# Kernel tuning notes

Measured on AMD Instinct MI355X. Metric: run time of the kernel, lower is better.

## Reference

```python
import jax, jax.numpy as jnp
import numpy as np

B, H, W, C, NH, WS, SS = 32, 56, 56, 128, 4, 7, 3
L = H * W
N = WS * WS
HD = C // NH
EPS = 1e-5


def _rel_pos_index():
    coords = np.stack(np.meshgrid(np.arange(WS), np.arange(WS), indexing='ij'))  # (2,ws,ws)
    flat = coords.reshape(2, -1)  # (2,N)
    rel = flat[:, :, None] - flat[:, None, :]  # (2,N,N)
    rel = rel.transpose(1, 2, 0).astype(np.int64)
    rel[..., 0] += WS - 1
    rel[..., 1] += WS - 1
    rel[..., 0] *= 2 * WS - 1
    return jnp.asarray(rel.sum(-1), dtype=jnp.int32)  # (N,N)


def setup_inputs() -> dict:
    key = jax.random.key(0)
    ks = jax.random.split(key, 8)
    s = 0.02
    return {
        'x': jax.random.normal(ks[0], (B, L, C), jnp.float32),
        'norm1_g': jnp.ones((C,), jnp.float32),
        'norm1_b': jnp.zeros((C,), jnp.float32),
        'qkv_w': jax.random.normal(ks[1], (3 * C, C), jnp.float32) * s,
        'qkv_b': jnp.zeros((3 * C,), jnp.float32),
        'rpb_table': jax.random.normal(ks[2], ((2 * WS - 1) ** 2, NH), jnp.float32) * s,
        'proj_w': jax.random.normal(ks[3], (C, C), jnp.float32) * s,
        'proj_b': jnp.zeros((C,), jnp.float32),
        'norm2_g': jnp.ones((C,), jnp.float32),
        'norm2_b': jnp.zeros((C,), jnp.float32),
        'fc1_w': jax.random.normal(ks[4], (4 * C, C), jnp.float32) * s,
        'fc1_b': jnp.zeros((4 * C,), jnp.float32),
        'fc2_w': jax.random.normal(ks[5], (C, 4 * C), jnp.float32) * s,
        'fc2_b': jnp.zeros((C,), jnp.float32),
        'rel_idx': _rel_pos_index(),
    }


def _ln(h, g, b):
    mu = jnp.mean(h, axis=-1, keepdims=True)
    var = jnp.mean((h - mu) ** 2, axis=-1, keepdims=True)
    return (h - mu) * jax.lax.rsqrt(var + EPS) * g + b


def reference(x, norm1_g, norm1_b, qkv_w, qkv_b, rpb_table, proj_w, proj_b,
              norm2_g, norm2_b, fc1_w, fc1_b, fc2_w, fc2_b, rel_idx):
    nHw, nWw = H // WS, W // WS
    scale = HD ** (-0.5)

    shortcut = x
    h = _ln(x, norm1_g, norm1_b).reshape(B, H, W, C)
    # cyclic shift
    h = jnp.roll(h, shift=(-SS, -SS), axis=(1, 2))
    # window partition -> (B*nW, N, C)
    w = h.reshape(B, nHw, WS, nWw, WS, C).transpose(0, 1, 3, 2, 4, 5)
    w = w.reshape(B * nHw * nWw, N, C)

    qkv = w @ qkv_w.T + qkv_b  # (Bw, N, 3C)
    q, k, v = jnp.split(qkv, 3, axis=-1)
    q = q.reshape(-1, N, NH, HD).transpose(0, 2, 1, 3)  # (Bw, nh, N, hd)
    k = k.reshape(-1, N, NH, HD).transpose(0, 2, 1, 3)
    v = v.reshape(-1, N, NH, HD).transpose(0, 2, 1, 3)

    attn = jnp.einsum('bhnd,bhmd->bhnm', q * scale, k)
    bias = rpb_table[rel_idx.reshape(-1)].reshape(N, N, NH).transpose(2, 0, 1)  # (nh,N,N)
    attn = jax.nn.softmax(attn + bias[None], axis=-1)

    out = jnp.einsum('bhnm,bhmd->bhnd', attn, v)
    out = out.transpose(0, 2, 1, 3).reshape(-1, N, C)
    out = out @ proj_w.T + proj_b

    # window reverse + un-shift
    out = out.reshape(B, nHw, nWw, WS, WS, C).transpose(0, 1, 3, 2, 4, 5)
    out = out.reshape(B, H, W, C)
    out = jnp.roll(out, shift=(SS, SS), axis=(1, 2)).reshape(B, L, C)

    x = shortcut + out
    h2 = _ln(x, norm2_g, norm2_b)
    mlp = jax.nn.gelu(h2 @ fc1_w.T + fc1_b, approximate=False) @ fc2_w.T + fc2_b
    return x + mlp
```

## Files before the change

### kernel.cpp

```cpp
#include <hip/hip_runtime.h>

typedef unsigned short ushort_t;
typedef unsigned int uint_t;

typedef __bf16 bf16x8 __attribute__((ext_vector_type(8)));
typedef float f32x4 __attribute__((ext_vector_type(4)));

static __device__ __forceinline__ float bf2f(ushort_t h) {
    return __uint_as_float(((uint_t)h) << 16);
}
static __device__ __forceinline__ ushort_t f2bf(float f) {
    uint_t u = __float_as_uint(f);
    u = u + 0x7FFFu + ((u >> 16) & 1u);
    return (ushort_t)(u >> 16);
}
static __device__ __forceinline__ uint_t pkbf(float lo, float hi) {
    uint_t a = __float_as_uint(lo) + 0x8000u;
    uint_t b = __float_as_uint(hi) + 0x8000u;
    return __builtin_amdgcn_perm(b, a, 0x07060302u);
}

#define BB 32
#define HH 56
#define WW_ 56
#define CC 128
#define NHEAD 4
#define WS 7
#define SS 3
#define LL (HH * WW_)
#define NTOK (BB * LL)
#define NWIN (BB * 64)
#define NN 49
#define HD 32
#define PLS 40
#define VTS 72

static __device__ __forceinline__ int win2tok(int wid) {
    int win = wid / NN, t = wid - win * NN;
    int bb = win >> 6, wrem = win & 63;
    int wi = wrem >> 3, wj = wrem & 7;
    int ti = t / WS, tj = t - ti * WS;
    int hh = wi * WS + ti + SS; if (hh >= HH) hh -= HH;
    int ww = wj * WS + tj + SS; if (ww >= WW_) ww -= WW_;
    return bb * LL + hh * WW_ + ww;
}

__global__ __launch_bounds__(256) void prep_all(
    const float* __restrict__ qkv_w, const float* __restrict__ proj_w,
    const float* __restrict__ fc1_w, const float* __restrict__ fc2_w,
    ushort_t* __restrict__ dst,
    const float* __restrict__ rpb, const int* __restrict__ rel_idx,
    float* __restrict__ bias) {
    int b = blockIdx.x;
    if (b < 768) {
        int i = b * 256 + threadIdx.x;
        const float* src;
        int off;
        if (i < 49152)        { src = qkv_w;  off = i; }
        else if (i < 65536)   { src = proj_w; off = i - 49152; }
        else if (i < 131072)  { src = fc1_w;  off = i - 65536; }
        else                  { src = fc2_w;  off = i - 131072; }
        dst[i] = f2bf(src[off]);
    } else {
        int h = b - 768;
        for (int idx = threadIdx.x; idx < 4096; idx += 256) {
            int i = idx >> 6, j = idx & 63;
            float v = 0.f;
            if (i < NN && j < NN)
                v = rpb[(size_t)rel_idx[i * NN + j] * NHEAD + h];
            bias[h * 4096 + idx] = v;
        }
    }
}

__global__ __launch_bounds__(256) void swin_fused(
    const float* __restrict__ x, const float* __restrict__ g1,
    const float* __restrict__ b1ln, const ushort_t* __restrict__ wq,
    const float* __restrict__ qkv_b, const float* __restrict__ bias,
    const ushort_t* __restrict__ wp, const float* __restrict__ proj_b,
    const float* __restrict__ g2, const float* __restrict__ b2,
    const ushort_t* __restrict__ w1, const float* __restrict__ fc1b,
    const ushort_t* __restrict__ w2, const float* __restrict__ bias2,
    float* __restrict__ out) {
    __shared__ __align__(16) ushort_t U[16384];
    __shared__ __align__(16) ushort_t HV[NHEAD][32 * VTS];
    __shared__ float MRm[64];
    __shared__ float MRs[64];
    const int tid = threadIdx.x;
    const int wave = tid >> 6;
    const int lane = tid & 63;
    const int l16 = lane & 15;
    const int quad = lane >> 4;
    const int h = wave;
    const int win = blockIdx.x;
    const int wn = wave * 32;
    const float scale = 0.17677669529663687f;

    ushort_t* XLN = U;
    char* QK = (char*)(U + h * 4096);
    ushort_t* PL = U + h * 4096;
    ushort_t* VT = HV[h];
    ushort_t* AH = U;
    ushort_t* PS = (ushort_t*)HV;

    {
        int row = tid >> 2;
        int ch0 = (tid & 3) * 32;
        int t = (row < NN) ? row : 0;
        int gtok = win2tok(win * NN + t);
        const float* xp = x + (size_t)gtok * CC + ch0;
        float v[32];
        float s = 0.f, sq = 0.f;
        #pragma unroll
        for (int i = 0; i < 4; ++i) {
            float4 a0 = *(const float4*)(xp + i * 8);
            float4 a1 = *(const float4*)(xp + i * 8 + 4);
            v[i * 8 + 0] = a0.x; v[i * 8 + 1] = a0.y;
            v[i * 8 + 2] = a0.z; v[i * 8 + 3] = a0.w;
            v[i * 8 + 4] = a1.x; v[i * 8 + 5] = a1.y;
            v[i * 8 + 6] = a1.z; v[i * 8 + 7] = a1.w;
            #pragma unroll
            for (int j = 0; j < 8; ++j) { s += v[i * 8 + j]; sq += v[i * 8 + j] * v[i * 8 + j]; }
        }
        s += __shfl_xor(s, 1);  sq += __shfl_xor(sq, 1);
        s += __shfl_xor(s, 2);  sq += __shfl_xor(sq, 2);
        float mean = s * (1.0f / 128.0f);
        float var = sq * (1.0f / 128.0f) - mean * mean;
        float rstd = rsqrtf(var + 1e-5f);
        #pragma unroll
        for (int i = 0; i < 4; ++i) {
            ushort_t tmp[8];
            #pragma unroll
            for (int j = 0; j < 8; ++j) {
                int c = ch0 + i * 8 + j;
                tmp[j] = f2bf((v[i * 8 + j] - mean) * rstd * g1[c] + b1ln[c]);
            }
            *(uint4*)&XLN[row * 136 + ch0 + i * 8] = *(const uint4*)tmp;
        }
    }
    __syncthreads();

    bf16x8 tf[4][4];
    #pragma unroll
    for (int kk = 0; kk < 4; ++kk)
        #pragma unroll
        for (int i = 0; i < 4; ++i)
            tf[kk][i] = *(const bf16x8*)&XLN[(16 * i + l16) * 136 + kk * 32 + quad * 8];
    __syncthreads();

    #pragma unroll
    for (int j = 0; j < 2; ++j) {
        f32x4 s1[4];
        #pragma unroll
        for (int i = 0; i < 4; ++i)
            s1[i] = (f32x4){0.f, 0.f, 0.f, 0.f};
        #pragma unroll
        for (int kk = 0; kk < 4; ++kk) {
            bf16x8 wf = *(const bf16x8*)&wq[(size_t)(h * 32 + 16 * j + l16) * 128 + kk * 32 + quad * 8];
            #pragma unroll
            for (int i = 0; i < 4; ++i)
                s1[i] = __builtin_amdgcn_mfma_f32_16x16x32_bf16(wf, tf[kk][i], s1[i], 0, 0, 0);
        }
        float4 bv = *(const float4*)&qkv_b[h * 32 + 16 * j + quad * 4];
        #pragma unroll
        for (int i = 0; i < 4; ++i) {
            uint2 pk;
            pk.x = pkbf((s1[i][0] + bv.x) * scale, (s1[i][1] + bv.y) * scale);
            pk.y = pkbf((s1[i][2] + bv.z) * scale, (s1[i][3] + bv.w) * scale);
            int row = 16 * i + l16;
            *(uint2*)(QK + row * 128 + ((32 * j + 8 * quad) ^ ((row & 7) << 4))) = pk;
        }
    }
    #pragma unroll
    for (int j = 0; j < 2; ++j) {
        f32x4 s1[4];
        #pragma unroll
        for (int i = 0; i < 4; ++i)
            s1[i] = (f32x4){0.f, 0.f, 0.f, 0.f};
        #pragma unroll
        for (int kk = 0; kk < 4; ++kk) {
            bf16x8 wf = *(const bf16x8*)&wq[(size_t)(128 + h * 32 + 16 * j + l16) * 128 + kk * 32 + quad * 8];
            #pragma unroll
            for (int i = 0; i < 4; ++i)
                s1[i] = __builtin_amdgcn_mfma_f32_16x16x32_bf16(wf, tf[kk][i], s1[i], 0, 0, 0);
        }
        float4 bv = *(const float4*)&qkv_b[128 + h * 32 + 16 * j + quad * 4];
        #pragma unroll
        for (int i = 0; i < 4; ++i) {
            uint2 pk;
            pk.x = pkbf(s1[i][0] + bv.x, s1[i][1] + bv.y);
            pk.y = pkbf(s1[i][2] + bv.z, s1[i][3] + bv.w);
            int row = 16 * i + l16;
            *(uint2*)(QK + row * 128 + ((64 + 32 * j + 8 * quad) ^ ((row & 7) << 4))) = pk;
        }
    }
    #pragma unroll
    for (int j = 0; j < 2; ++j) {
        f32x4 sv[4];
        #pragma unroll
        for (int i = 0; i < 4; ++i)
            sv[i] = (f32x4){0.f, 0.f, 0.f, 0.f};
        #pragma unroll
        for (int kk = 0; kk < 4; ++kk) {
            bf16x8 wf = *(const bf16x8*)&wq[(size_t)(256 + h * 32 + 16 * j + l16) * 128 + kk * 32 + quad * 8];
            #pragma unroll
            for (int i = 0; i < 4; ++i)
                sv[i] = __builtin_amdgcn_mfma_f32_16x16x32_bf16(tf[kk][i], wf, sv[i], 0, 0, 0);
        }
        float bvv = qkv_b[256 + h * 32 + 16 * j + l16];
        #pragma unroll
        for (int i = 0; i < 4; ++i) {
            uint2 pk;
            pk.x = pkbf(sv[i][0] + bvv, sv[i][1] + bvv);
            pk.y = pkbf(sv[i][2] + bvv, sv[i][3] + bvv);
            *(uint2*)&VT[(16 * j + l16) * VTS + 16 * i + quad * 4] = pk;
        }
    }

    f32x4 s[4][4];
    {
        bf16x8 qa[4], kb[4];
        #pragma unroll
        for (int t = 0; t < 4; ++t) {
            int row = 16 * t + l16;
            int swz = (row & 7) << 4;
            qa[t] = *(const bf16x8*)(QK + row * 128 + ((16 * quad) ^ swz));
            kb[t] = *(const bf16x8*)(QK + row * 128 + ((64 + 16 * quad) ^ swz));
        }
        #pragma unroll
        for (int mi = 0; mi < 4; ++mi)
            #pragma unroll
            for (int ni = 0; ni < 4; ++ni) {
                f32x4 z = {0.f, 0.f, 0.f, 0.f};
                s[mi][ni] = __builtin_amdgcn_mfma_f32_16x16x32_bf16(qa[mi], kb[ni], z, 0, 0, 0);
            }
    }

    const float* bh = bias + h * 4096;
    #pragma unroll
    for (int mi = 0; mi < 4; ++mi)
        #pragma unroll
        for (int ni = 0; ni < 4; ++ni)
            #pragma unroll
            for (int r = 0; r < 4; ++r)
                s[mi][ni][r] += bh[(16 * mi + quad * 4 + r) * 64 + 16 * ni + l16];

    #pragma unroll
    for (int mi = 0; mi < 4; ++mi)
        #pragma unroll
        for (int r = 0; r < 4; ++r) {
            float e0 = __expf(s[mi][0][r]);
            float e1 = __expf(s[mi][1][r]);
            float e2 = __expf(s[mi][2][r]);
            float e3 = (l16 == 0) ? __expf(s[mi][3][r]) : 0.f;
            float sum = (e0 + e1) + (e2 + e3);
            sum += __shfl_xor(sum, 1);
            sum += __shfl_xor(sum, 2);
            sum += __shfl_xor(sum, 4);
            sum += __shfl_xor(sum, 8);
            float inv = __builtin_amdgcn_rcpf(sum);
            s[mi][0][r] = e0 * inv;
            s[mi][1][r] = e1 * inv;
            s[mi][2][r] = e2 * inv;
            s[mi][3][r] = e3 * inv;
        }

    uint2 pP[4][4];
    #pragma unroll
    for (int mi = 0; mi < 4; ++mi)
        #pragma unroll
        for (int ni = 0; ni < 4; ++ni) {
            pP[mi][ni].x = pkbf(s[mi][ni][0], s[mi][ni][1]);
            pP[mi][ni].y = pkbf(s[mi][ni][2], s[mi][ni][3]);
        }

    f32x4 o[2][4];
    #pragma unroll
    for (int k0 = 0; k0 < 64; k0 += 32) {
        int nb = k0 >> 4;
        #pragma unroll
        for (int mi = 0; mi < 4; ++mi)
            #pragma unroll
            for (int nn = 0; nn < 2; ++nn) {
                uint2 pk = pP[mi][nb + nn];
                int base = (16 * mi + quad * 4) * PLS + 16 * nn + l16;
                PL[base] = (ushort_t)pk.x;
                PL[base + PLS] = (ushort_t)(pk.x >> 16);
                PL[base + 2 * PLS] = (ushort_t)pk.y;
                PL[base + 3 * PLS] = (ushort_t)(pk.y >> 16);
            }
        bf16x8 va[2], pb[4];
        #pragma unroll
        for (int it = 0; it < 2; ++it)
            va[it] = *(const bf16x8*)&VT[(16 * it + l16) * VTS + k0 + quad * 8];
        #pragma unroll
        for (int jt = 0; jt < 4; ++jt)
            pb[jt] = *(const bf16x8*)&PL[(16 * jt + l16) * PLS + quad * 8];
        #pragma unroll
        for (int it = 0; it < 2; ++it)
            #pragma unroll
            for (int jt = 0; jt < 4; ++jt) {
                if (k0 == 0) {
                    f32x4 z = {0.f, 0.f, 0.f, 0.f};
                    o[it][jt] = __builtin_amdgcn_mfma_f32_16x16x32_bf16(va[it], pb[jt], z, 0, 0, 0);
                } else {
                    o[it][jt] = __builtin_amdgcn_mfma_f32_16x16x32_bf16(va[it], pb[jt], o[it][jt], 0, 0, 0);
                }
            }
    }
    __syncthreads();

    #pragma unroll
    for (int jt = 0; jt < 4; ++jt) {
        int m = 16 * jt + l16;
        #pragma unroll
        for (int it = 0; it < 2; ++it) {
            ushort4 st;
            st.x = f2bf(o[it][jt][0]);
            st.y = f2bf(o[it][jt][1]);
            st.z = f2bf(o[it][jt][2]);
            st.w = f2bf(o[it][jt][3]);
            *(ushort4*)&AH[m * 136 + h * HD + 16 * it + quad * 4] = st;
        }
    }
    __syncthreads();

    {
        f32x4 pa[2][4];
        #pragma unroll
        for (int j = 0; j < 2; ++j)
            #pragma unroll
            for (int i = 0; i < 4; ++i)
                pa[j][i] = (f32x4){0.f, 0.f, 0.f, 0.f};
        #pragma unroll
        for (int kk = 0; kk < 4; ++kk) {
            bf16x8 af[4];
            #pragma unroll
            for (int i = 0; i < 4; ++i)
                af[i] = *(const bf16x8*)&AH[(16 * i + l16) * 136 + kk * 32 + quad * 8];
            #pragma unroll
            for (int j = 0; j < 2; ++j) {
                bf16x8 wf = *(const bf16x8*)&wp[(size_t)(wn + 16 * j + l16) * 128 + kk * 32 + quad * 8];
                #pragma unroll
                for (int i = 0; i < 4; ++i)
                    pa[j][i] = __builtin_amdgcn_mfma_f32_16x16x32_bf16(wf, af[i], pa[j][i], 0, 0, 0);
            }
        }
        #pragma unroll
        for (int j = 0; j < 2; ++j) {
            float4 bv = *(const float4*)&proj_b[wn + 16 * j + quad * 4];
            #pragma unroll
            for (int i = 0; i < 4; ++i) {
                uint2 pk;
                pk.x = pkbf(pa[j][i][0] + bv.x, pa[j][i][1] + bv.y);
                pk.y = pkbf(pa[j][i][2] + bv.z, pa[j][i][3] + bv.w);
                *(uint2*)&PS[(16 * i + l16) * 136 + wn + 16 * j + quad * 4] = pk;
            }
        }
    }
    __syncthreads();

    {
        int row = tid >> 2;
        int ch0 = (tid & 3) * 32;
        int t = (row < NN) ? row : 0;
        int gtok = win2tok(win * NN + t);
        const float* xp = x + (size_t)gtok * CC + ch0;
        float v[32];
        float s2 = 0.f, sq = 0.f;
        #pragma unroll
        for (int i = 0; i < 4; ++i) {
            float4 a0 = *(const float4*)(xp + i * 8);
            float4 a1 = *(const float4*)(xp + i * 8 + 4);
            ushort4 p0 = *(const ushort4*)&PS[row * 136 + ch0 + i * 8];
            ushort4 p1 = *(const ushort4*)&PS[row * 136 + ch0 + i * 8 + 4];
            v[i * 8 + 0] = a0.x + bf2f(p0.x); v[i * 8 + 1] = a0.y + bf2f(p0.y);
            v[i * 8 + 2] = a0.z + bf2f(p0.z); v[i * 8 + 3] = a0.w + bf2f(p0.w);
            v[i * 8 + 4] = a1.x + bf2f(p1.x); v[i * 8 + 5] = a1.y + bf2f(p1.y);
            v[i * 8 + 6] = a1.z + bf2f(p1.z); v[i * 8 + 7] = a1.w + bf2f(p1.w);
            #pragma unroll
            for (int j = 0; j < 8; ++j) { s2 += v[i * 8 + j]; sq += v[i * 8 + j] * v[i * 8 + j]; }
        }
        s2 += __shfl_xor(s2, 1);  sq += __shfl_xor(sq, 1);
        s2 += __shfl_xor(s2, 2);  sq += __shfl_xor(sq, 2);
        float mean = s2 * (1.0f / 128.0f);
        float var = sq * (1.0f / 128.0f) - mean * mean;
        float rstd = rsqrtf(var + 1e-5f);
        if ((tid & 3) == 0) {
            MRm[row] = mean;
            MRs[row] = (var + 1e-5f) * rstd;
        }
        #pragma unroll
        for (int i = 0; i < 4; ++i) {
            ushort_t tmp[8];
            #pragma unroll
            for (int j = 0; j < 8; ++j) {
                int c = ch0 + i * 8 + j;
                tmp[j] = f2bf((v[i * 8 + j] - mean) * rstd * g2[c] + b2[c]);
            }
            *(uint4*)&AH[row * 136 + ch0 + i * 8] = *(const uint4*)tmp;
        }
    }
    __syncthreads();

    f32x4 acc2[2][4];
    #pragma unroll
    for (int j = 0; j < 2; ++j)
        #pragma unroll
        for (int i = 0; i < 4; ++i)
            acc2[j][i] = (f32x4){0.f, 0.f, 0.f, 0.f};

    for (int c = 0; c < 4; ++c) {
        f32x4 s1[2][4];
        #pragma unroll
        for (int j = 0; j < 2; ++j)
            #pragma unroll
            for (int i = 0; i < 4; ++i)
                s1[j][i] = (f32x4){0.f, 0.f, 0.f, 0.f};
        #pragma unroll
        for (int kk = 0; kk < 4; ++kk) {
            bf16x8 hf[4];
            #pragma unroll
            for (int i = 0; i < 4; ++i)
                hf[i] = *(const bf16x8*)&AH[(16 * i + l16) * 136 + kk * 32 + quad * 8];
            #pragma unroll
            for (int j = 0; j < 2; ++j) {
                bf16x8 wf = *(const bf16x8*)&w1[(size_t)(c * 128 + wn + 16 * j + l16) * 128 + kk * 32 + quad * 8];
                #pragma unroll
                for (int i = 0; i < 4; ++i)
                    s1[j][i] = __builtin_amdgcn_mfma_f32_16x16x32_bf16(wf, hf[i], s1[j][i], 0, 0, 0);
            }
        }
        uint2 pk[2][4];
        #pragma unroll
        for (int j = 0; j < 2; ++j) {
            float4 bv = *(const float4*)&fc1b[c * 128 + wn + 16 * j + quad * 4];
            #pragma unroll
            for (int i = 0; i < 4; ++i) {
                float g[4];
                #pragma unroll
                for (int r = 0; r < 4; ++r) {
                    float u = s1[j][i][r] + ((const float*)&bv)[r];
                    float u2 = u * u;
                    float z = u * __builtin_fmaf(0.0713548163f, u2, 1.5957691216f);
                    float e = __expf(-z);
                    g[r] = u * __builtin_amdgcn_rcpf(1.0f + e);
                }
                pk[j][i].x = pkbf(g[0], g[1]);
                pk[j][i].y = pkbf(g[2], g[3]);
            }
        }
        __syncthreads();
        #pragma unroll
        for (int j = 0; j < 2; ++j)
            #pragma unroll
            for (int i = 0; i < 4; ++i)
                *(uint2*)&PS[(16 * i + l16) * 136 + wn + 16 * j + quad * 4] = pk[j][i];
        __syncthreads();
        #pragma unroll
        for (int kk = 0; kk < 4; ++kk) {
            bf16x8 pf[4];
            #pragma unroll
            for (int i = 0; i < 4; ++i)
                pf[i] = *(const bf16x8*)&PS[(16 * i + l16) * 136 + kk * 32 + quad * 8];
            #pragma unroll
            for (int j = 0; j < 2; ++j) {
                bf16x8 wf = *(const bf16x8*)&w2[(size_t)(wn + 16 * j + l16) * 512 + c * 128 + kk * 32 + quad * 8];
                #pragma unroll
                for (int i = 0; i < 4; ++i)
                    acc2[j][i] = __builtin_amdgcn_mfma_f32_16x16x32_bf16(wf, pf[i], acc2[j][i], 0, 0, 0);
            }
        }
    }

    float invg[2][4], b2v[2][4];
    #pragma unroll
    for (int j = 0; j < 2; ++j) {
        float4 gv = *(const float4*)&g2[wn + 16 * j + quad * 4];
        float4 bv = *(const float4*)&b2[wn + 16 * j + quad * 4];
        invg[j][0] = __builtin_amdgcn_rcpf(gv.x);
        invg[j][1] = __builtin_amdgcn_rcpf(gv.y);
        invg[j][2] = __builtin_amdgcn_rcpf(gv.z);
        invg[j][3] = __builtin_amdgcn_rcpf(gv.w);
        b2v[j][0] = bv.x; b2v[j][1] = bv.y; b2v[j][2] = bv.z; b2v[j][3] = bv.w;
    }
    #pragma unroll
    for (int i = 0; i < 4; ++i) {
        int row = 16 * i + l16;
        if (row < NN) {
            int gtok = win2tok(win * NN + row);
            float mean = MRm[row];
            float sd = MRs[row];
            #pragma unroll
            for (int j = 0; j < 2; ++j) {
                float4 bb = *(const float4*)&bias2[wn + 16 * j + quad * 4];
                ushort4 hv = *(const ushort4*)&AH[row * 136 + wn + 16 * j + quad * 4];
                float4 cur;
                cur.x = (bf2f(hv.x) - b2v[j][0]) * (invg[j][0] * sd) + mean + acc2[j][i][0] + bb.x;
                cur.y = (bf2f(hv.y) - b2v[j][1]) * (invg[j][1] * sd) + mean + acc2[j][i][1] + bb.y;
                cur.z = (bf2f(hv.z) - b2v[j][2]) * (invg[j][2] * sd) + mean + acc2[j][i][2] + bb.z;
                cur.w = (bf2f(hv.w) - b2v[j][3]) * (invg[j][3] * sd) + mean + acc2[j][i][3] + bb.w;
                *(float4*)(out + (size_t)gtok * CC + wn + 16 * j + quad * 4) = cur;
            }
        }
    }
}

extern "C" void kernel_launch(void* const* d_in, const int* in_sizes, int n_in,
                              void* d_out, int out_size, void* d_ws, size_t ws_size,
                              hipStream_t stream) {
    const float* x       = (const float*)d_in[0];
    const float* norm1_g = (const float*)d_in[1];
    const float* norm1_b = (const float*)d_in[2];
    const float* qkv_w   = (const float*)d_in[3];
    const float* qkv_b   = (const float*)d_in[4];
    const float* rpb     = (const float*)d_in[5];
    const float* proj_w  = (const float*)d_in[6];
    const float* proj_b  = (const float*)d_in[7];
    const float* norm2_g = (const float*)d_in[8];
    const float* norm2_b = (const float*)d_in[9];
    const float* fc1_w   = (const float*)d_in[10];
    const float* fc1_b   = (const float*)d_in[11];
    const float* fc2_w   = (const float*)d_in[12];
    const float* fc2_b   = (const float*)d_in[13];
    const int*   rel_idx = (const int*)d_in[14];

    char* ws = (char*)d_ws;
    float*    biasT = (float*)ws;
    ushort_t* wall  = (ushort_t*)(ws + 65536);
    ushort_t* wqkv  = wall;
    ushort_t* wproj = wall + 49152;
    ushort_t* wfc1  = wall + 65536;
    ushort_t* wfc2  = wall + 131072;

    prep_all<<<dim3(772), dim3(256), 0, stream>>>(
        qkv_w, proj_w, fc1_w, fc2_w, wall, rpb, rel_idx, biasT);
    swin_fused<<<dim3(NWIN), dim3(256), 0, stream>>>(
        x, norm1_g, norm1_b, wqkv, qkv_b, biasT,
        wproj, proj_b, norm2_g, norm2_b,
        wfc1, fc1_b, wfc2, fc2_b, (float*)d_out);
}
```

Before: 271.5 us.

## Keep V in registers via ds_bpermute, shrink LDS pool, target 4 blocks/CU

```diff
diff --git a/kernel.cpp b/kernel.cpp
--- a/kernel.cpp
+++ b/kernel.cpp
@@ -33,7 +33,6 @@
 #define NN 49
 #define HD 32
 #define PLS 40
-#define VTS 72
 
 static __device__ __forceinline__ int win2tok(int wid) {
     int win = wid / NN, t = wid - win * NN;
@@ -73,7 +72,7 @@
     }
 }
 
-__global__ __launch_bounds__(256) void swin_fused(
+__global__ __launch_bounds__(256, 4) void swin_fused(
     const float* __restrict__ x, const float* __restrict__ g1,
     const float* __restrict__ b1ln, const ushort_t* __restrict__ wq,
     const float* __restrict__ qkv_b, const float* __restrict__ bias,
@@ -82,8 +81,7 @@
     const ushort_t* __restrict__ w1, const float* __restrict__ fc1b,
     const ushort_t* __restrict__ w2, const float* __restrict__ bias2,
     float* __restrict__ out) {
-    __shared__ __align__(16) ushort_t U[16384];
-    __shared__ __align__(16) ushort_t HV[NHEAD][32 * VTS];
+    __shared__ __align__(16) ushort_t POOL[17408];
     __shared__ float MRm[64];
     __shared__ float MRs[64];
     const int tid = threadIdx.x;
@@ -96,12 +94,11 @@
     const int wn = wave * 32;
     const float scale = 0.17677669529663687f;
 
-    ushort_t* XLN = U;
-    char* QK = (char*)(U + h * 4096);
-    ushort_t* PL = U + h * 4096;
-    ushort_t* VT = HV[h];
-    ushort_t* AH = U;
-    ushort_t* PS = (ushort_t*)HV;
+    ushort_t* XLN = POOL;
+    char* QK = (char*)POOL + h * 8192;
+    ushort_t* PL = POOL + h * 4096;
+    ushort_t* AH = POOL;
+    ushort_t* PS = POOL + 8704;
 
     {
         int row = tid >> 2;
@@ -148,6 +145,28 @@
             tf[kk][i] = *(const bf16x8*)&XLN[(16 * i + l16) * 136 + kk * 32 + quad * 8];
     __syncthreads();
 
+    uint2 pv[2][4];
+    #pragma unroll
+    for (int j = 0; j < 2; ++j) {
+        f32x4 sv[4];
+        #pragma unroll
+        for (int i = 0; i < 4; ++i)
+            sv[i] = (f32x4){0.f, 0.f, 0.f, 0.f};
+        #pragma unroll
+        for (int kk = 0; kk < 4; ++kk) {
+            bf16x8 wf = *(const bf16x8*)&wq[(size_t)(256 + h * 32 + 16 * j + l16) * 128 + kk * 32 + quad * 8];
+            #pragma unroll
+            for (int i = 0; i < 4; ++i)
+                sv[i] = __builtin_amdgcn_mfma_f32_16x16x32_bf16(tf[kk][i], wf, sv[i], 0, 0, 0);
+        }
+        float bvv = qkv_b[256 + h * 32 + 16 * j + l16];
+        #pragma unroll
+        for (int i = 0; i < 4; ++i) {
+            pv[j][i].x = pkbf(sv[i][0] + bvv, sv[i][1] + bvv);
+            pv[j][i].y = pkbf(sv[i][2] + bvv, sv[i][3] + bvv);
+        }
+    }
+
     #pragma unroll
     for (int j = 0; j < 2; ++j) {
         f32x4 s1[4];
@@ -194,119 +213,110 @@
             *(uint2*)(QK + row * 128 + ((64 + 32 * j + 8 * quad) ^ ((row & 7) << 4))) = pk;
         }
     }
-    #pragma unroll
-    for (int j = 0; j < 2; ++j) {
-        f32x4 sv[4];
-        #pragma unroll
-        for (int i = 0; i < 4; ++i)
-            sv[i] = (f32x4){0.f, 0.f, 0.f, 0.f};
-        #pragma unroll
-        for (int kk = 0; kk < 4; ++kk) {
-            bf16x8 wf = *(const bf16x8*)&wq[(size_t)(256 + h * 32 + 16 * j + l16) * 128 + kk * 32 + quad * 8];
-            #pragma unroll
-            for (int i = 0; i < 4; ++i)
-                sv[i] = __builtin_amdgcn_mfma_f32_16x16x32_bf16(tf[kk][i], wf, sv[i], 0, 0, 0);
-        }
-        float bvv = qkv_b[256 + h * 32 + 16 * j + l16];
-        #pragma unroll
-        for (int i = 0; i < 4; ++i) {
-            uint2 pk;
-            pk.x = pkbf(sv[i][0] + bvv, sv[i][1] + bvv);
-            pk.y = pkbf(sv[i][2] + bvv, sv[i][3] + bvv);
-            *(uint2*)&VT[(16 * j + l16) * VTS + 16 * i + quad * 4] = pk;
-        }
-    }
-
-    f32x4 s[4][4];
+
+    uint2 pP[4][4];
     {
-        bf16x8 qa[4], kb[4];
+        bf16x8 kb[4];
         #pragma unroll
         for (int t = 0; t < 4; ++t) {
             int row = 16 * t + l16;
             int swz = (row & 7) << 4;
-            qa[t] = *(const bf16x8*)(QK + row * 128 + ((16 * quad) ^ swz));
             kb[t] = *(const bf16x8*)(QK + row * 128 + ((64 + 16 * quad) ^ swz));
         }
-        #pragma unroll
-        for (int mi = 0; mi < 4; ++mi)
+        const float* bh = bias + h * 4096;
+        #pragma unroll
+        for (int mi = 0; mi < 4; ++mi) {
+            int qrow = 16 * mi + l16;
+            int qswz = (qrow & 7) << 4;
+            bf16x8 qa = *(const bf16x8*)(QK + qrow * 128 + ((16 * quad) ^ qswz));
+            f32x4 sm[4];
             #pragma unroll
             for (int ni = 0; ni < 4; ++ni) {
                 f32x4 z = {0.f, 0.f, 0.f, 0.f};
-                s[mi][ni] = __builtin_amdgcn_mfma_f32_16x16x32_bf16(qa[mi], kb[ni], z, 0, 0, 0);
-            }
-    }
-
-    const float* bh = bias + h * 4096;
-    #pragma unroll
-    for (int mi = 0; mi < 4; ++mi)
-        #pragma unroll
-        for (int ni = 0; ni < 4; ++ni)
-            #pragma unroll
-            for (int r = 0; r < 4; ++r)
-                s[mi][ni][r] += bh[(16 * mi + quad * 4 + r) * 64 + 16 * ni + l16];
-
-    #pragma unroll
-    for (int mi = 0; mi < 4; ++mi)
-        #pragma unroll
-        for (int r = 0; r < 4; ++r) {
-            float e0 = __expf(s[mi][0][r]);
-            float e1 = __expf(s[mi][1][r]);
-            float e2 = __expf(s[mi][2][r]);
-            float e3 = (l16 == 0) ? __expf(s[mi][3][r]) : 0.f;
-            float sum = (e0 + e1) + (e2 + e3);
-            sum += __shfl_xor(sum, 1);
-            sum += __shfl_xor(sum, 2);
-            sum += __shfl_xor(sum, 4);
-            sum += __shfl_xor(sum, 8);
-            float inv = __builtin_amdgcn_rcpf(sum);
-            s[mi][0][r] = e0 * inv;
-            s[mi][1][r] = e1 * inv;
-            s[mi][2][r] = e2 * inv;
-            s[mi][3][r] = e3 * inv;
-        }
-
-    uint2 pP[4][4];
-    #pragma unroll
-    for (int mi = 0; mi < 4; ++mi)
-        #pragma unroll
-        for (int ni = 0; ni < 4; ++ni) {
-            pP[mi][ni].x = pkbf(s[mi][ni][0], s[mi][ni][1]);
-            pP[mi][ni].y = pkbf(s[mi][ni][2], s[mi][ni][3]);
-        }
+                sm[ni] = __builtin_amdgcn_mfma_f32_16x16x32_bf16(qa, kb[ni], z, 0, 0, 0);
+            }
+            #pragma unroll
+            for (int ni = 0; ni < 4; ++ni)
+                #pragma unroll
+                for (int r = 0; r < 4; ++r)
+                    sm[ni][r] += bh[(16 * mi + quad * 4 + r) * 64 + 16 * ni + l16];
+            #pragma unroll
+            for (int r = 0; r < 4; ++r) {
+                float e0 = __expf(sm[0][r]);
+                float e1 = __expf(sm[1][r]);
+                float e2 = __expf(sm[2][r]);
+                float e3 = (l16 == 0) ? __expf(sm[3][r]) : 0.f;
+                float sum = (e0 + e1) + (e2 + e3);
+                sum += __shfl_xor(sum, 1);
+                sum += __shfl_xor(sum, 2);
+                sum += __shfl_xor(sum, 4);
+                sum += __shfl_xor(sum, 8);
+                float inv = __builtin_amdgcn_rcpf(sum);
+                sm[0][r] = e0 * inv;
+                sm[1][r] = e1 * inv;
+                sm[2][r] = e2 * inv;
+                sm[3][r] = e3 * inv;
+            }
+            #pragma unroll
+            for (int ni = 0; ni < 4; ++ni) {
+                pP[mi][ni].x = pkbf(sm[ni][0], sm[ni][1]);
+                pP[mi][ni].y = pkbf(sm[ni][2], sm[ni][3]);
+            }
+        }
+    }
 
     f32x4 o[2][4];
-    #pragma unroll
-    for (int k0 = 0; k0 < 64; k0 += 32) {
-        int nb = k0 >> 4;
-        #pragma unroll
-        for (int mi = 0; mi < 4; ++mi)
-            #pragma unroll
-            for (int nn = 0; nn < 2; ++nn) {
-                uint2 pk = pP[mi][nb + nn];
-                int base = (16 * mi + quad * 4) * PLS + 16 * nn + l16;
-                PL[base] = (ushort_t)pk.x;
-                PL[base + PLS] = (ushort_t)(pk.x >> 16);
-                PL[base + 2 * PLS] = (ushort_t)pk.y;
-                PL[base + 3 * PLS] = (ushort_t)(pk.y >> 16);
-            }
-        bf16x8 va[2], pb[4];
-        #pragma unroll
-        for (int it = 0; it < 2; ++it)
-            va[it] = *(const bf16x8*)&VT[(16 * it + l16) * VTS + k0 + quad * 8];
-        #pragma unroll
-        for (int jt = 0; jt < 4; ++jt)
-            pb[jt] = *(const bf16x8*)&PL[(16 * jt + l16) * PLS + quad * 8];
-        #pragma unroll
-        for (int it = 0; it < 2; ++it)
-            #pragma unroll
-            for (int jt = 0; jt < 4; ++jt) {
-                if (k0 == 0) {
-                    f32x4 z = {0.f, 0.f, 0.f, 0.f};
-                    o[it][jt] = __builtin_amdgcn_mfma_f32_16x16x32_bf16(va[it], pb[jt], z, 0, 0, 0);
-                } else {
-                    o[it][jt] = __builtin_amdgcn_mfma_f32_16x16x32_bf16(va[it], pb[jt], o[it][jt], 0, 0, 0);
+    {
+        int la = (l16 + 16 * ((2 * quad) & 3)) << 2;
+        int lb = (l16 + 16 * ((2 * quad + 1) & 3)) << 2;
+        bool hiQ = (quad & 2) != 0;
+        #pragma unroll
+        for (int k0 = 0; k0 < 64; k0 += 32) {
+            int nb = k0 >> 4;
+            #pragma unroll
+            for (int mi = 0; mi < 4; ++mi)
+                #pragma unroll
+                for (int nn = 0; nn < 2; ++nn) {
+                    uint2 pk = pP[mi][nb + nn];
+                    int base = (16 * mi + quad * 4) * PLS + 16 * nn + l16;
+                    PL[base] = (ushort_t)pk.x;
+                    PL[base + PLS] = (ushort_t)(pk.x >> 16);
+                    PL[base + 2 * PLS] = (ushort_t)pk.y;
+                    PL[base + 3 * PLS] = (ushort_t)(pk.y >> 16);
                 }
-            }
+            bf16x8 va[2], pb[4];
+            #pragma unroll
+            for (int it = 0; it < 2; ++it) {
+                uint_t c0x = (uint_t)__builtin_amdgcn_ds_bpermute(la, (int)pv[it][nb].x);
+                uint_t c1x = (uint_t)__builtin_amdgcn_ds_bpermute(la, (int)pv[it][nb + 1].x);
+                uint_t c0y = (uint_t)__builtin_amdgcn_ds_bpermute(la, (int)pv[it][nb].y);
+                uint_t c1y = (uint_t)__builtin_amdgcn_ds_bpermute(la, (int)pv[it][nb + 1].y);
+                uint_t d0x = (uint_t)__builtin_amdgcn_ds_bpermute(lb, (int)pv[it][nb].x);
+                uint_t d1x = (uint_t)__builtin_amdgcn_ds_bpermute(lb, (int)pv[it][nb + 1].x);
+                uint_t d0y = (uint_t)__builtin_amdgcn_ds_bpermute(lb, (int)pv[it][nb].y);
+                uint_t d1y = (uint_t)__builtin_amdgcn_ds_bpermute(lb, (int)pv[it][nb + 1].y);
+                uint4 u;
+                u.x = hiQ ? c1x : c0x;
+                u.y = hiQ ? c1y : c0y;
+                u.z = hiQ ? d1x : d0x;
+                u.w = hiQ ? d1y : d0y;
+                va[it] = *(bf16x8*)&u;
+            }
+            #pragma unroll
+            for (int jt = 0; jt < 4; ++jt)
+                pb[jt] = *(const bf16x8*)&PL[(16 * jt + l16) * PLS + quad * 8];
+            #pragma unroll
+            for (int it = 0; it < 2; ++it)
+                #pragma unroll
+                for (int jt = 0; jt < 4; ++jt) {
+                    if (k0 == 0) {
+                        f32x4 z = {0.f, 0.f, 0.f, 0.f};
+                        o[it][jt] = __builtin_amdgcn_mfma_f32_16x16x32_bf16(va[it], pb[jt], z, 0, 0, 0);
+                    } else {
+                        o[it][jt] = __builtin_amdgcn_mfma_f32_16x16x32_bf16(va[it], pb[jt], o[it][jt], 0, 0, 0);
+                    }
+                }
+        }
     }
     __syncthreads();
 
```

Result: slower. 302.5 us (+11.4%).
